# Optimization experiments

Hardware: AMD Instinct MI355X
Metric: run time of the kernel (lower is better)

## Reference

```python
import jax, jax.numpy as jnp
import numpy as np

N = 16000
E = 512000
HID = 128
OUT = 64
BN_EPS = 1e-5


def setup_inputs() -> dict:
    key = jax.random.key(0)
    ks = jax.random.split(key, 8)
    x = jax.random.normal(ks[0], (N, HID), dtype=jnp.float32)
    src = jax.random.randint(ks[1], (E,), 0, N, dtype=jnp.int32)
    dst = jax.random.randint(ks[2], (E,), 0, N, dtype=jnp.int32)
    s = 1.0 / np.sqrt(HID)
    fc_w = jax.random.uniform(ks[3], (OUT, HID), jnp.float32, -s, s)
    fc_b = jnp.zeros((OUT,), jnp.float32)
    w1 = jax.random.uniform(ks[4], (HID, HID), jnp.float32, -s, s)
    b1 = jnp.zeros((HID,), jnp.float32)
    w2 = jax.random.uniform(ks[5], (OUT, HID), jnp.float32, -s, s)
    b2 = jnp.zeros((OUT,), jnp.float32)
    epsilon = jnp.full((N,), 0.5, jnp.float32)
    gamma = jnp.ones((OUT,), jnp.float32)
    beta = jnp.zeros((OUT,), jnp.float32)
    return {"x": x, "src": src, "dst": dst, "fc_w": fc_w, "fc_b": fc_b,
            "w1": w1, "b1": b1, "w2": w2, "b2": b2,
            "epsilon": epsilon, "gamma": gamma, "beta": beta}


def _agg(feat, src, dst, n):
    # DGL update_all(copy_src, sum): gather source features, scatter-sum to dst.
    return jax.ops.segment_sum(feat[src], dst, num_segments=n)


def reference(x, src, dst, fc_w, fc_b, w1, b1, w2, b2, epsilon, gamma, beta):
    n = x.shape[0]
    # skip-path linear projection
    h1 = x @ fc_w.T + fc_b                       # [N, OUT]
    # GraphConv layer 1: aggregate then linear, then ReLU
    h2 = jax.nn.relu(_agg(x, src, dst, n) @ w1.T + b1)   # [N, HID]
    # GraphConv layer 2
    h2 = _agg(h2, src, dst, n) @ w2.T + b2       # [N, OUT]
    # per-node epsilon blend
    eps = epsilon[:, None]
    h = (1.0 - eps) * h1 + eps * h2              # [N, OUT]
    # averaged gram matrices
    ret = (h @ h.T + x @ x.T) * 0.5              # [N, N]
    # BatchNorm1d (training mode: biased batch stats)
    mean = jnp.mean(h, axis=0)
    var = jnp.mean(jnp.square(h - mean), axis=0)
    hn = (h - mean) * jax.lax.rsqrt(var + BN_EPS) * gamma + beta
    return ret, hn
```

## Files before the change

### kernel.cpp

```cpp
#include <hip/hip_runtime.h>
#include <hip/hip_bf16.h>

typedef __bf16 bf16x8 __attribute__((ext_vector_type(8)));
typedef float  f32x4  __attribute__((ext_vector_type(4)));
typedef unsigned short u16x8 __attribute__((ext_vector_type(8)));

#define HID 128
#define OUT 64
#define BN_EPS 1e-5f

__device__ __forceinline__ float bf2f(unsigned short u) {
  union { unsigned int i; float f; } c; c.i = ((unsigned)u) << 16; return c.f;
}

__global__ __launch_bounds__(256) void xconv_k(
    const float* __restrict__ x, unsigned short* __restrict__ xbf,
    int* __restrict__ cnt, int n)
{
  int gid = blockIdx.x * blockDim.x + threadIdx.x;
  if (gid < n) cnt[gid] = 0;
  int stride = gridDim.x * blockDim.x;
  int total = n * 32;
  for (int idx = gid; idx < total; idx += stride) {
    f32x4 v = ((const f32x4*)x)[idx];
    ushort4 o;
    __bf16 b0 = (__bf16)v[0], b1 = (__bf16)v[1], b2 = (__bf16)v[2], b3 = (__bf16)v[3];
    o.x = *(unsigned short*)&b0; o.y = *(unsigned short*)&b1;
    o.z = *(unsigned short*)&b2; o.w = *(unsigned short*)&b3;
    ((ushort4*)xbf)[idx] = o;
  }
}

__global__ __launch_bounds__(256) void hist_k(
    const int* __restrict__ dst, int* __restrict__ cnt, int e)
{
  int stride = gridDim.x * blockDim.x;
  for (int i = blockIdx.x * blockDim.x + threadIdx.x; i < e; i += stride)
    atomicAdd(&cnt[dst[i]], 1);
}

__global__ __launch_bounds__(256) void scan_k(
    const int* __restrict__ cnt, int* __restrict__ offsets,
    int* __restrict__ cursor, float* __restrict__ stats, int n)
{
  int t = threadIdx.x;
  if (t < 128) stats[t] = 0.f;
  __shared__ int part[256];
  int chunk = (n + 255) / 256;
  int base = t * chunk;
  int s = 0;
  for (int i = 0; i < chunk; ++i) {
    int idx = base + i;
    if (idx < n) s += cnt[idx];
  }
  part[t] = s;
  __syncthreads();
  for (int off = 1; off < 256; off <<= 1) {
    int v = 0;
    if (t >= off) v = part[t - off];
    __syncthreads();
    if (t >= off) part[t] += v;
    __syncthreads();
  }
  int run = (t == 0) ? 0 : part[t - 1];
  for (int i = 0; i < chunk; ++i) {
    int idx = base + i;
    if (idx < n) {
      offsets[idx] = run;
      cursor[idx]  = run;
      run += cnt[idx];
    }
  }
  if (t == 255) offsets[n] = run;
}

__global__ __launch_bounds__(256) void place_k(
    const int* __restrict__ src, const int* __restrict__ dst,
    int* __restrict__ cursor, int* __restrict__ sorted_src, int e)
{
  int stride = gridDim.x * blockDim.x;
  for (int i = blockIdx.x * blockDim.x + threadIdx.x; i < e; i += stride) {
    int pos = atomicAdd(&cursor[dst[i]], 1);
    sorted_src[pos] = src[i];
  }
}

__global__ __launch_bounds__(256) void aggx_k(
    const unsigned short* __restrict__ xbf, const int* __restrict__ sorted_src,
    const int* __restrict__ offsets, float* __restrict__ agg, int n)
{
  int wave = (blockIdx.x * 256 + threadIdx.x) >> 6;
  int lane = threadIdx.x & 63;
  if (wave >= n) return;
  int qtr = lane >> 4;
  int l16 = lane & 15;
  int beg = offsets[wave], end = offsets[wave + 1];
  float a0[8] = {}, a1[8] = {};
  int i = beg + qtr;
  for (; i + 4 < end; i += 8) {
    int s0 = sorted_src[i];
    int s1 = sorted_src[i + 4];
    u16x8 v0 = *(const u16x8*)(xbf + (size_t)s0 * HID + l16 * 8);
    u16x8 v1 = *(const u16x8*)(xbf + (size_t)s1 * HID + l16 * 8);
    #pragma unroll
    for (int j = 0; j < 8; ++j) { a0[j] += bf2f(v0[j]); a1[j] += bf2f(v1[j]); }
  }
  if (i < end) {
    int s0 = sorted_src[i];
    u16x8 v0 = *(const u16x8*)(xbf + (size_t)s0 * HID + l16 * 8);
    #pragma unroll
    for (int j = 0; j < 8; ++j) a0[j] += bf2f(v0[j]);
  }
  #pragma unroll
  for (int j = 0; j < 8; ++j) a0[j] += a1[j];
  #pragma unroll
  for (int j = 0; j < 8; ++j) a0[j] += __shfl_xor(a0[j], 16, 64);
  #pragma unroll
  for (int j = 0; j < 8; ++j) a0[j] += __shfl_xor(a0[j], 32, 64);
  if (qtr == 0) {
    f32x4 lo = {a0[0], a0[1], a0[2], a0[3]};
    f32x4 hi = {a0[4], a0[5], a0[6], a0[7]};
    *(f32x4*)(agg + (size_t)wave * HID + l16 * 8)     = lo;
    *(f32x4*)(agg + (size_t)wave * HID + l16 * 8 + 4) = hi;
  }
}

__global__ __launch_bounds__(256) void agg2y_k(
    const unsigned short* __restrict__ y2, const int* __restrict__ sorted_src,
    const int* __restrict__ offsets, float* __restrict__ aggy, int n)
{
  int wave = (blockIdx.x * 256 + threadIdx.x) >> 6;
  int lane = threadIdx.x & 63;
  if (wave >= n) return;
  int qtr = lane >> 4;
  int l16 = lane & 15;
  int beg = offsets[wave], end = offsets[wave + 1];
  f32x4 a0 = {0.f, 0.f, 0.f, 0.f}, a1 = {0.f, 0.f, 0.f, 0.f};
  int i = beg + qtr;
  for (; i + 4 < end; i += 8) {
    int s0 = sorted_src[i];
    int s1 = sorted_src[i + 4];
    ushort4 v0 = *(const ushort4*)(y2 + (size_t)s0 * OUT + l16 * 4);
    ushort4 v1 = *(const ushort4*)(y2 + (size_t)s1 * OUT + l16 * 4);
    a0[0] += bf2f(v0.x); a0[1] += bf2f(v0.y); a0[2] += bf2f(v0.z); a0[3] += bf2f(v0.w);
    a1[0] += bf2f(v1.x); a1[1] += bf2f(v1.y); a1[2] += bf2f(v1.z); a1[3] += bf2f(v1.w);
  }
  if (i < end) {
    int s0 = sorted_src[i];
    ushort4 v0 = *(const ushort4*)(y2 + (size_t)s0 * OUT + l16 * 4);
    a0[0] += bf2f(v0.x); a0[1] += bf2f(v0.y); a0[2] += bf2f(v0.z); a0[3] += bf2f(v0.w);
  }
  a0 += a1;
  f32x4 other;
  #pragma unroll
  for (int j = 0; j < 4; ++j) other[j] = __shfl_xor(a0[j], 16, 64);
  a0 += other;
  #pragma unroll
  for (int j = 0; j < 4; ++j) other[j] = __shfl_xor(a0[j], 32, 64);
  a0 += other;
  if (qtr == 0)
    *(f32x4*)(aggy + (size_t)wave * OUT + l16 * 4) = a0;
}

__global__ __launch_bounds__(256) void mlp_fused_k(
    const float* __restrict__ agg, const float* __restrict__ w1,
    const float* __restrict__ b1, const float* __restrict__ w2,
    unsigned short* __restrict__ y2, int n)
{
  __shared__ float aggs[16][132];
  __shared__ float h2s[16][132];
  int t = threadIdx.x;
  int rbase = blockIdx.x * 16;

  for (int idx = t; idx < 16 * 32; idx += 256) {
    int r = idx >> 5, c = idx & 31;
    ((f32x4*)&aggs[r][0])[c] = ((const f32x4*)(agg + (size_t)(rbase + r) * HID))[c];
  }
  __syncthreads();

  {
    int j = t & 127, rh = t >> 7;
    const f32x4* w1r = (const f32x4*)(w1 + (size_t)j * HID);
    float acc[8];
    float bj = b1[j];
    #pragma unroll
    for (int p = 0; p < 8; ++p) acc[p] = bj;
    for (int k = 0; k < 32; ++k) {
      f32x4 w = w1r[k];
      #pragma unroll
      for (int p = 0; p < 8; ++p) {
        f32x4 a = ((const f32x4*)&aggs[rh * 8 + p][0])[k];
        acc[p] += w[0] * a[0] + w[1] * a[1] + w[2] * a[2] + w[3] * a[3];
      }
    }
    #pragma unroll
    for (int p = 0; p < 8; ++p) h2s[rh * 8 + p][j] = fmaxf(acc[p], 0.f);
  }
  __syncthreads();

  {
    int o = t & 63, rq = t >> 6;
    const f32x4* w2r = (const f32x4*)(w2 + (size_t)o * HID);
    float acc[4] = {0.f, 0.f, 0.f, 0.f};
    for (int k = 0; k < 32; ++k) {
      f32x4 w = w2r[k];
      #pragma unroll
      for (int p = 0; p < 4; ++p) {
        f32x4 a = ((const f32x4*)&h2s[rq + p * 4][0])[k];
        acc[p] += w[0] * a[0] + w[1] * a[1] + w[2] * a[2] + w[3] * a[3];
      }
    }
    #pragma unroll
    for (int p = 0; p < 4; ++p) {
      __bf16 b = (__bf16)acc[p];
      y2[(size_t)(rbase + rq + p * 4) * OUT + o] = *(unsigned short*)&b;
    }
  }
}

__global__ __launch_bounds__(256) void combine_k(
    const float* __restrict__ x, const float* __restrict__ aggy,
    const float* __restrict__ fcw, const float* __restrict__ fcb,
    const float* __restrict__ b2,
    const float* __restrict__ eps, float* __restrict__ h,
    unsigned short* __restrict__ hbf, float* __restrict__ stats, int n)
{
  __shared__ float xs[32][132];
  __shared__ float ls[256], lss[256];
  int t = threadIdx.x;
  int rbase = blockIdx.x * 32;

  for (int idx = t; idx < 32 * 32; idx += 256) {
    int r = idx >> 5, c = idx & 31;
    ((f32x4*)&xs[r][0])[c] = ((const f32x4*)(x + (size_t)(rbase + r) * HID))[c];
  }
  __syncthreads();

  int o = t & 63, rq = t >> 6;
  const f32x4* fwr = (const f32x4*)(fcw + (size_t)o * HID);
  float fb = fcb[o], bb = b2[o];
  float acc[8];
  #pragma unroll
  for (int p = 0; p < 8; ++p) acc[p] = fb;
  for (int k = 0; k < 32; ++k) {
    f32x4 w = fwr[k];
    #pragma unroll
    for (int p = 0; p < 8; ++p) {
      f32x4 a = ((const f32x4*)&xs[rq + p * 4][0])[k];
      acc[p] += w[0] * a[0] + w[1] * a[1] + w[2] * a[2] + w[3] * a[3];
    }
  }
  float s = 0.f, ss = 0.f;
  #pragma unroll
  for (int p = 0; p < 8; ++p) {
    int row = rbase + rq + p * 4;
    float a2 = aggy[(size_t)row * OUT + o] + bb;
    float ev = eps[row];
    float hv = (1.f - ev) * acc[p] + ev * a2;
    h[(size_t)row * OUT + o] = hv;
    __bf16 hb = (__bf16)hv;
    hbf[(size_t)row * OUT + o] = *(unsigned short*)&hb;
    s += hv; ss += hv * hv;
  }
  ls[t] = s; lss[t] = ss;
  __syncthreads();
  if (t < 64) {
    s  = ls[t]  + ls[t + 64]  + ls[t + 128]  + ls[t + 192];
    ss = lss[t] + lss[t + 64] + lss[t + 128] + lss[t + 192];
    atomicAdd(&stats[t], s);
    atomicAdd(&stats[64 + t], ss);
  }
}

__global__ __launch_bounds__(256) void hn_k(
    const float* __restrict__ h, const float* __restrict__ stats,
    const float* __restrict__ gamma, const float* __restrict__ beta,
    float* __restrict__ outp, int n)
{
  int stride = gridDim.x * blockDim.x;
  int total  = n * OUT;
  float inv_n = 1.f / (float)n;
  for (int idx = blockIdx.x * blockDim.x + threadIdx.x; idx < total; idx += stride) {
    int col = idx & 63;
    float mean = stats[col] * inv_n;
    float var  = stats[64 + col] * inv_n - mean * mean;
    float sc   = rsqrtf(var + BN_EPS) * gamma[col];
    outp[idx] = (h[idx] - mean) * sc + beta[col];
  }
}

__global__ __launch_bounds__(256, 3) void gemm_k(
    const unsigned short* __restrict__ hbf, const unsigned short* __restrict__ xbf,
    float* __restrict__ out, int n, int nwg)
{
  __shared__ char pool[64 * 132 * 4];
  __bf16* As = (__bf16*)pool;
  __bf16* Bs = (__bf16*)(pool + 16384);
  float*  T  = (float*)pool;

  int nb = n >> 7;
  int orig = blockIdx.x;
  int q = nwg >> 3, r = nwg & 7;
  int xcd = orig & 7, idx8 = orig >> 3;
  int bid = (xcd < r ? xcd * (q + 1) : r * (q + 1) + (xcd - r) * q) + idx8;

  int bi = 0, rem = bid;
  while (rem >= nb - bi) { rem -= nb - bi; ++bi; }
  int bj = bi + rem;
  int t = threadIdx.x;
  int w = t >> 6, lane = t & 63;
  int wr = (w >> 1) << 6;
  int wc = (w & 1) << 6;
  int lr = lane & 15, lg = lane >> 4;

  const uint4* ha = (const uint4*)(hbf + (size_t)bi * 128 * OUT);
  const uint4* hb = (const uint4*)(hbf + (size_t)bj * 128 * OUT);
  const uint4* xa = (const uint4*)(xbf + (size_t)bi * 128 * HID);
  const uint4* xb = (const uint4*)(xbf + (size_t)bj * 128 * HID);
  uint4* Asv = (uint4*)As;
  uint4* Bsv = (uint4*)Bs;

  f32x4 acc[4][4] = {};
  #pragma unroll
  for (int kc = 0; kc < 3; ++kc) {
    #pragma unroll
    for (int it = 0; it < 4; ++it) {
      int ch = t + it * 256;
      int row = ch >> 3, c = ch & 7;
      int sw = row * 8 + (c ^ (row & 7));
      uint4 va, vb;
      if (kc == 0) { va = ha[row * 8 + c];                  vb = hb[row * 8 + c]; }
      else         { va = xa[row * 16 + (kc - 1) * 8 + c];  vb = xb[row * 16 + (kc - 1) * 8 + c]; }
      Asv[sw] = va;
      Bsv[sw] = vb;
    }
    __syncthreads();
    const bf16x8* Ac = (const bf16x8*)As;
    const bf16x8* Bc = (const bf16x8*)Bs;
    #pragma unroll
    for (int ks = 0; ks < 2; ++ks) {
      bf16x8 a[4], b[4];
      #pragma unroll
      for (int m = 0; m < 4; ++m) {
        int ar = wr + m * 16 + lr;
        int br = wc + m * 16 + lr;
        a[m] = Ac[ar * 8 + ((ks * 4 + lg) ^ (ar & 7))];
        b[m] = Bc[br * 8 + ((ks * 4 + lg) ^ (br & 7))];
      }
      #pragma unroll
      for (int m = 0; m < 4; ++m)
        #pragma unroll
        for (int nn = 0; nn < 4; ++nn)
          acc[m][nn] = __builtin_amdgcn_mfma_f32_16x16x32_bf16(a[m], b[nn], acc[m][nn], 0, 0, 0);
    }
    __syncthreads();
  }

  #pragma unroll
  for (int m = 0; m < 4; ++m)
    #pragma unroll
    for (int nn = 0; nn < 4; ++nn)
      acc[m][nn] = acc[m][nn] * 0.5f;

  size_t N = (size_t)n;

  if (bi != bj) {
    #pragma unroll
    for (int p = 0; p < 2; ++p) {
      if ((wc >> 6) == p) {
        #pragma unroll
        for (int m = 0; m < 4; ++m)
          #pragma unroll
          for (int nn = 0; nn < 4; ++nn) {
            int c  = nn * 16 + lr;
            int r0 = wr + m * 16 + lg * 4;
            *(f32x4*)&T[c * 132 + r0] = acc[m][nn];
          }
      }
      __syncthreads();
      #pragma unroll
      for (int it = 0; it < 8; ++it) {
        int idx = t + it * 256;
        int rr = idx >> 5, c4 = idx & 31;
        f32x4 v = *(const f32x4*)&T[rr * 132 + c4 * 4];
        *(f32x4*)&out[(size_t)(bj * 128 + p * 64 + rr) * N + bi * 128 + c4 * 4] = v;
      }
      __syncthreads();
    }
  }

  #pragma unroll
  for (int m = 0; m < 4; ++m) {
    size_t gr0 = (size_t)(bi * 128 + wr + m * 16 + lg * 4);
    #pragma unroll
    for (int nn = 0; nn < 4; ++nn) {
      int gc = bj * 128 + wc + nn * 16 + lr;
      #pragma unroll
      for (int r = 0; r < 4; ++r)
        out[(gr0 + r) * N + gc] = acc[m][nn][r];
    }
  }
}

extern "C" void kernel_launch(void* const* d_in, const int* in_sizes, int n_in,
                              void* d_out, int out_size, void* d_ws, size_t ws_size,
                              hipStream_t stream) {
  const float* x    = (const float*)d_in[0];
  const int*   src  = (const int*)d_in[1];
  const int*   dst  = (const int*)d_in[2];
  const float* fcw  = (const float*)d_in[3];
  const float* fcb  = (const float*)d_in[4];
  const float* w1   = (const float*)d_in[5];
  const float* b1   = (const float*)d_in[6];
  const float* w2   = (const float*)d_in[7];
  const float* b2   = (const float*)d_in[8];
  const float* eps  = (const float*)d_in[9];
  const float* gamma= (const float*)d_in[10];
  const float* beta = (const float*)d_in[11];
  int n = in_sizes[0] / HID;
  int e = in_sizes[1];
  float* out = (float*)d_out;

  char* ws = (char*)d_ws;
  size_t off = 0;
  float* agg   = (float*)(ws + off); off += (size_t)n * HID * 4;
  float* h     = (float*)(ws + off); off += (size_t)n * OUT * 4;
  float* aggy  = (float*)(ws + off); off += (size_t)n * OUT * 4;
  unsigned short* xbf = (unsigned short*)(ws + off); off += (size_t)n * HID * 2;
  unsigned short* hbf = (unsigned short*)(ws + off); off += (size_t)n * OUT * 2;
  unsigned short* y2  = (unsigned short*)(ws + off); off += (size_t)n * OUT * 2;
  float* stats = (float*)(ws + off); off += 512;
  int* cnt     = (int*)(ws + off); off += (size_t)n * 4;
  int* offsets = (int*)(ws + off); off += (size_t)(n + 1) * 4;
  int* cursor  = (int*)(ws + off); off += (size_t)n * 4;
  int* sorted_src = (int*)(ws + off); off += (size_t)e * 4;

  xconv_k<<<2048, 256, 0, stream>>>(x, xbf, cnt, n);
  hist_k<<<512, 256, 0, stream>>>(dst, cnt, e);
  scan_k<<<1, 256, 0, stream>>>(cnt, offsets, cursor, stats, n);
  place_k<<<512, 256, 0, stream>>>(src, dst, cursor, sorted_src, e);

  aggx_k<<<(n * 64 + 255) / 256, 256, 0, stream>>>(xbf, sorted_src, offsets, agg, n);
  mlp_fused_k<<<n / 16, 256, 0, stream>>>(agg, w1, b1, w2, y2, n);
  agg2y_k<<<(n * 64 + 255) / 256, 256, 0, stream>>>(y2, sorted_src, offsets, aggy, n);
  combine_k<<<n / 32, 256, 0, stream>>>(x, aggy, fcw, fcb, b2, eps, h, hbf, stats, n);
  hn_k<<<1024, 256, 0, stream>>>(h, stats, gamma, beta, out + (size_t)n * n, n);

  int nb = n >> 7;
  int nwg = nb * (nb + 1) / 2;
  gemm_k<<<nwg, 256, 0, stream>>>(hbf, xbf, out, n, nwg);
}
```

Measured before the change: 398.6 us.

## Fuse histogram into convert kernel, widen scan, use 16-bit sorted indices, unroll gathers

Merges the bf16 conversion and degree histogram into one prep kernel and zeroes the counts with a memset instead of inside the kernel. The single-block scan now runs with 1024 threads. Sorted source indices are stored as 16-bit values, halving index traffic, which only works while N is at most 65536. The gather loops in both aggregation kernels are unrolled to three in-flight rows for more memory-level parallelism, at the cost of extra registers.

```diff
diff --git a/kernel.cpp b/kernel.cpp
--- a/kernel.cpp
+++ b/kernel.cpp
@@ -13,12 +13,11 @@
   union { unsigned int i; float f; } c; c.i = ((unsigned)u) << 16; return c.f;
 }
 
-__global__ __launch_bounds__(256) void xconv_k(
+__global__ __launch_bounds__(256) void prep_k(
     const float* __restrict__ x, unsigned short* __restrict__ xbf,
-    int* __restrict__ cnt, int n)
+    const int* __restrict__ dst, int* __restrict__ cnt, int n, int e)
 {
   int gid = blockIdx.x * blockDim.x + threadIdx.x;
-  if (gid < n) cnt[gid] = 0;
   int stride = gridDim.x * blockDim.x;
   int total = n * 32;
   for (int idx = gid; idx < total; idx += stride) {
@@ -29,24 +28,18 @@
     o.z = *(unsigned short*)&b2; o.w = *(unsigned short*)&b3;
     ((ushort4*)xbf)[idx] = o;
   }
-}
-
-__global__ __launch_bounds__(256) void hist_k(
-    const int* __restrict__ dst, int* __restrict__ cnt, int e)
-{
-  int stride = gridDim.x * blockDim.x;
-  for (int i = blockIdx.x * blockDim.x + threadIdx.x; i < e; i += stride)
+  for (int i = gid; i < e; i += stride)
     atomicAdd(&cnt[dst[i]], 1);
 }
 
-__global__ __launch_bounds__(256) void scan_k(
+__global__ __launch_bounds__(1024) void scan_k(
     const int* __restrict__ cnt, int* __restrict__ offsets,
     int* __restrict__ cursor, float* __restrict__ stats, int n)
 {
   int t = threadIdx.x;
   if (t < 128) stats[t] = 0.f;
-  __shared__ int part[256];
-  int chunk = (n + 255) / 256;
+  __shared__ int part[1024];
+  int chunk = (n + 1023) / 1024;
   int base = t * chunk;
   int s = 0;
   for (int i = 0; i < chunk; ++i) {
@@ -55,7 +48,7 @@
   }
   part[t] = s;
   __syncthreads();
-  for (int off = 1; off < 256; off <<= 1) {
+  for (int off = 1; off < 1024; off <<= 1) {
     int v = 0;
     if (t >= off) v = part[t - off];
     __syncthreads();
@@ -71,22 +64,22 @@
       run += cnt[idx];
     }
   }
-  if (t == 255) offsets[n] = run;
+  if (t == 1023) offsets[n] = run;
 }
 
 __global__ __launch_bounds__(256) void place_k(
     const int* __restrict__ src, const int* __restrict__ dst,
-    int* __restrict__ cursor, int* __restrict__ sorted_src, int e)
+    int* __restrict__ cursor, unsigned short* __restrict__ sorted_src, int e)
 {
   int stride = gridDim.x * blockDim.x;
   for (int i = blockIdx.x * blockDim.x + threadIdx.x; i < e; i += stride) {
     int pos = atomicAdd(&cursor[dst[i]], 1);
-    sorted_src[pos] = src[i];
+    sorted_src[pos] = (unsigned short)src[i];
   }
 }
 
 __global__ __launch_bounds__(256) void aggx_k(
-    const unsigned short* __restrict__ xbf, const int* __restrict__ sorted_src,
+    const unsigned short* __restrict__ xbf, const unsigned short* __restrict__ sorted_src,
     const int* __restrict__ offsets, float* __restrict__ agg, int n)
 {
   int wave = (blockIdx.x * 256 + threadIdx.x) >> 6;
@@ -95,24 +88,26 @@
   int qtr = lane >> 4;
   int l16 = lane & 15;
   int beg = offsets[wave], end = offsets[wave + 1];
-  float a0[8] = {}, a1[8] = {};
+  float a0[8] = {}, a1[8] = {}, a2[8] = {};
   int i = beg + qtr;
-  for (; i + 4 < end; i += 8) {
+  for (; i + 8 < end; i += 12) {
     int s0 = sorted_src[i];
     int s1 = sorted_src[i + 4];
+    int s2 = sorted_src[i + 8];
     u16x8 v0 = *(const u16x8*)(xbf + (size_t)s0 * HID + l16 * 8);
     u16x8 v1 = *(const u16x8*)(xbf + (size_t)s1 * HID + l16 * 8);
-    #pragma unroll
-    for (int j = 0; j < 8; ++j) { a0[j] += bf2f(v0[j]); a1[j] += bf2f(v1[j]); }
-  }
-  if (i < end) {
+    u16x8 v2 = *(const u16x8*)(xbf + (size_t)s2 * HID + l16 * 8);
+    #pragma unroll
+    for (int j = 0; j < 8; ++j) { a0[j] += bf2f(v0[j]); a1[j] += bf2f(v1[j]); a2[j] += bf2f(v2[j]); }
+  }
+  for (; i < end; i += 4) {
     int s0 = sorted_src[i];
     u16x8 v0 = *(const u16x8*)(xbf + (size_t)s0 * HID + l16 * 8);
     #pragma unroll
     for (int j = 0; j < 8; ++j) a0[j] += bf2f(v0[j]);
   }
   #pragma unroll
-  for (int j = 0; j < 8; ++j) a0[j] += a1[j];
+  for (int j = 0; j < 8; ++j) a0[j] += a1[j] + a2[j];
   #pragma unroll
   for (int j = 0; j < 8; ++j) a0[j] += __shfl_xor(a0[j], 16, 64);
   #pragma unroll
@@ -126,7 +121,7 @@
 }
 
 __global__ __launch_bounds__(256) void agg2y_k(
-    const unsigned short* __restrict__ y2, const int* __restrict__ sorted_src,
+    const unsigned short* __restrict__ y2, const unsigned short* __restrict__ sorted_src,
     const int* __restrict__ offsets, float* __restrict__ aggy, int n)
 {
   int wave = (blockIdx.x * 256 + threadIdx.x) >> 6;
@@ -135,22 +130,25 @@
   int qtr = lane >> 4;
   int l16 = lane & 15;
   int beg = offsets[wave], end = offsets[wave + 1];
-  f32x4 a0 = {0.f, 0.f, 0.f, 0.f}, a1 = {0.f, 0.f, 0.f, 0.f};
+  f32x4 a0 = {0.f, 0.f, 0.f, 0.f}, a1 = {0.f, 0.f, 0.f, 0.f}, a2 = {0.f, 0.f, 0.f, 0.f};
   int i = beg + qtr;
-  for (; i + 4 < end; i += 8) {
+  for (; i + 8 < end; i += 12) {
     int s0 = sorted_src[i];
     int s1 = sorted_src[i + 4];
+    int s2 = sorted_src[i + 8];
     ushort4 v0 = *(const ushort4*)(y2 + (size_t)s0 * OUT + l16 * 4);
     ushort4 v1 = *(const ushort4*)(y2 + (size_t)s1 * OUT + l16 * 4);
+    ushort4 v2 = *(const ushort4*)(y2 + (size_t)s2 * OUT + l16 * 4);
     a0[0] += bf2f(v0.x); a0[1] += bf2f(v0.y); a0[2] += bf2f(v0.z); a0[3] += bf2f(v0.w);
     a1[0] += bf2f(v1.x); a1[1] += bf2f(v1.y); a1[2] += bf2f(v1.z); a1[3] += bf2f(v1.w);
-  }
-  if (i < end) {
+    a2[0] += bf2f(v2.x); a2[1] += bf2f(v2.y); a2[2] += bf2f(v2.z); a2[3] += bf2f(v2.w);
+  }
+  for (; i < end; i += 4) {
     int s0 = sorted_src[i];
     ushort4 v0 = *(const ushort4*)(y2 + (size_t)s0 * OUT + l16 * 4);
     a0[0] += bf2f(v0.x); a0[1] += bf2f(v0.y); a0[2] += bf2f(v0.z); a0[3] += bf2f(v0.w);
   }
-  a0 += a1;
+  a0 += a1; a0 += a2;
   f32x4 other;
   #pragma unroll
   for (int j = 0; j < 4; ++j) other[j] = __shfl_xor(a0[j], 16, 64);
@@ -433,11 +431,12 @@
   int* cnt     = (int*)(ws + off); off += (size_t)n * 4;
   int* offsets = (int*)(ws + off); off += (size_t)(n + 1) * 4;
   int* cursor  = (int*)(ws + off); off += (size_t)n * 4;
-  int* sorted_src = (int*)(ws + off); off += (size_t)e * 4;
-
-  xconv_k<<<2048, 256, 0, stream>>>(x, xbf, cnt, n);
-  hist_k<<<512, 256, 0, stream>>>(dst, cnt, e);
-  scan_k<<<1, 256, 0, stream>>>(cnt, offsets, cursor, stats, n);
+  unsigned short* sorted_src = (unsigned short*)(ws + off); off += (size_t)e * 2;
+
+  hipMemsetAsync(cnt, 0, (size_t)n * 4, stream);
+
+  prep_k<<<2048, 256, 0, stream>>>(x, xbf, dst, cnt, n, e);
+  scan_k<<<1, 1024, 0, stream>>>(cnt, offsets, cursor, stats, n);
   place_k<<<512, 256, 0, stream>>>(src, dst, cursor, sorted_src, e);
 
   aggx_k<<<(n * 64 + 255) / 256, 256, 0, stream>>>(xbf, sorted_src, offsets, agg, n);
```

Result: no change. 393.3 us (-1.3%).
